# Optimization experiments

Hardware: AMD Instinct MI355X
Metric: run time of the kernel (lower is better)

## Reference

```python
import jax, jax.numpy as jnp
import numpy as np

N = 4096            # nodes
LMAX = 6
NUM_COEF = (LMAX + 1) ** 2   # 49 SH coefficients
RES = 18            # S2 grid resolution (lat = lon = 18)
C = 128             # num_channels


def setup_inputs() -> dict:
    key = jax.random.key(0)
    k1, k2, k3, k4 = jax.random.split(key, 4)
    return {
        "inputs": jax.random.normal(k1, (N, NUM_COEF, 2 * C), dtype=jnp.float32),
        "scalars": jax.random.normal(k2, (N, 3 * C), dtype=jnp.float32),
        # SO3Grid projection matrices (precomputed SH-basis grids in the real module)
        "to_grid_mat": jax.random.normal(k3, (RES, RES, NUM_COEF), dtype=jnp.float32) / np.sqrt(NUM_COEF).astype(np.float32),
        "from_grid_mat": jax.random.normal(k4, (RES, RES, NUM_COEF), dtype=jnp.float32) / np.float32(RES),
    }


def reference(inputs, scalars, to_grid_mat, from_grid_mat):
    # inputs:  [N, (lmax+1)^2, 2C]; scalars: [N, 3C]
    n, k, c2 = inputs.shape
    s = scalars[:, None, :]                       # [N, 1, 3C]
    # Type-0 path part 1: SwiGLU on first 2C scalars -> [N, 1, C]
    a, b = jnp.split(s[..., :c2], 2, axis=-1)
    output_scalars = jax.nn.silu(a) * b
    # Type-0 path part 2: sigmoid gate on last C scalars -> [N, 1, C]
    gate_scalars = jax.nn.sigmoid(s[..., c2:])
    # Type-L path: project to S2 grid -> [N, RES, RES, 2C]
    x_grid = jnp.einsum('pqi,nic->npqc', to_grid_mat, inputs)
    # chunk-multiply gating (self tensor product) -> [N, RES, RES, C]
    x1, x2 = jnp.split(x_grid, 2, axis=-1)
    x_grid = x1 * x2
    # project back to SH coefficients -> [N, (lmax+1)^2, C]
    output_vectors = jnp.einsum('pqi,npqc->nic', from_grid_mat, x_grid)
    output_vectors = output_vectors * gate_scalars
    # merge: add SwiGLU scalars onto the l=0 component
    return output_vectors.at[:, 0:1, :].add(output_scalars)
```

## Files before the change

### kernel.cpp

```cpp
#include <hip/hip_runtime.h>


#define KC    49
#define PQ    324
#define NPX   12544
#define OUTK  6272
#define NTILE 11
#define TROWS 325
#define TCOLS 68
#define FROWS 50
#define FCOLS 356
#define TTOT  (TROWS * TCOLS)
#define FTOT  (FROWS * FCOLS)
#define WTOT  (TTOT + FTOT)
#define WPAD  39904

typedef __attribute__((ext_vector_type(8)))  short bf16x8;
typedef __attribute__((ext_vector_type(4)))  short bf16x4;
typedef __attribute__((ext_vector_type(16))) float f32x16;
typedef __attribute__((ext_vector_type(4)))  unsigned int u32x4;

__device__ __forceinline__ unsigned int cvtpk_bf16(float lo, float hi) {
    unsigned int r;
    asm("v_cvt_pk_bf16_f32 %0, %1, %2" : "=v"(r) : "v"(lo), "v"(hi));
    return r;
}
__device__ __forceinline__ unsigned short f2bf(float f) {
    unsigned u = __builtin_bit_cast(unsigned, f);
    return (unsigned short)((u + 0x7FFFu + ((u >> 16) & 1u)) >> 16);
}
__device__ __forceinline__ bf16x8 ld8(const unsigned short* p) {
    const bf16x4 lo = *(const bf16x4*)p;
    const bf16x4 hi = *(const bf16x4*)(p + 4);
    bf16x8 r;
    r[0] = lo[0]; r[1] = lo[1]; r[2] = lo[2]; r[3] = lo[3];
    r[4] = hi[0]; r[5] = hi[1]; r[6] = hi[2]; r[7] = hi[3];
    return r;
}
__device__ __forceinline__ void load_ch(const float* xp, int xi, int st, int hb, float* buf) {
#pragma unroll
    for (int j = 0; j < 8; ++j) {
        const int i = 16 * st + 8 * hb + j;
        buf[j] = (i < KC) ? xp[128 * xi + (size_t)i * 256] : 0.0f;
    }
}
__device__ __forceinline__ bf16x8 cvt_ch(const float* buf) {
    u32x4 d;
#pragma unroll
    for (int p = 0; p < 4; ++p) d[p] = cvtpk_bf16(buf[2 * p], buf[2 * p + 1]);
    return __builtin_bit_cast(bf16x8, d);
}

__global__ void prep_kernel(const float* __restrict__ Tg, const float* __restrict__ Fg,
                            unsigned short* __restrict__ W)
{
    const int idx = blockIdx.x * 256 + threadIdx.x;
    if (idx < TTOT) {
        const int r = idx / TCOLS, i = idx % TCOLS;
        const float v = (r < PQ && i < KC) ? Tg[r * KC + i] : 0.0f;
        W[idx] = f2bf(v);
    } else if (idx < WPAD) {
        float v = 0.0f;
        if (idx < WTOT) {
            const int idx2 = idx - TTOT;
            const int k = idx2 / FCOLS, p = idx2 % FCOLS;
            if (k < KC && p < PQ) v = Fg[p * KC + k];
        }
        W[idx] = f2bf(v);
    }
}

__global__ __launch_bounds__(512, 4)
void s2_fused(const float* __restrict__ X,
              const float* __restrict__ S,
              const unsigned short* __restrict__ W,
              float* __restrict__ out,
              int nit)
{
    __shared__ __align__(16) unsigned short lds[WPAD];

    const int tid = threadIdx.x;
    for (int idx = tid; idx < WPAD / 8; idx += 512) {
        const u32x4 v = *(const u32x4*)(W + (size_t)idx * 8);
        *(u32x4*)(lds + (size_t)idx * 8) = v;
    }
    __syncthreads();

    const int w  = tid >> 6;
    const int l  = tid & 63;
    const int cl = l & 31;
    const int hb = l >> 5;
    const int cs = w >> 1;
    const int nw = w & 1;

    const unsigned short* tw  = lds;
    const unsigned short* fw0 = lds + TTOT + (size_t)cl * FCOLS;
    const unsigned short* fw1 = lds + TTOT + (size_t)min(cl + 32, KC) * FCOLS;

    const int nbase = blockIdx.x * (2 * nit) + nw;

    for (int it = 0; it < nit; ++it) {
        const int n = nbase + 2 * it;

        const float* xp = X + (size_t)n * NPX + 32 * cs + cl;
        const float* sp = S + (size_t)n * 384 + 32 * cs + cl;
        const float sraw0 = sp[0], sraw1 = sp[128], sraw2 = sp[256];
        const float sg  = 1.0f / (1.0f + __expf(-sraw2));
        const float osc = (sraw0 / (1.0f + __expf(-sraw0))) * sraw1;

        bf16x8 bx[2][4];
        {
            float rA[8], rB[8];
            load_ch(xp, 0, 0, hb, rA);
            load_ch(xp, 1, 0, hb, rB);
            bx[0][0] = cvt_ch(rA); load_ch(xp, 0, 1, hb, rA);
            bx[1][0] = cvt_ch(rB); load_ch(xp, 1, 1, hb, rB);
            bx[0][1] = cvt_ch(rA); load_ch(xp, 0, 2, hb, rA);
            bx[1][1] = cvt_ch(rB); load_ch(xp, 1, 2, hb, rB);
            bx[0][2] = cvt_ch(rA); load_ch(xp, 0, 3, hb, rA);
            bx[1][2] = cvt_ch(rB); load_ch(xp, 1, 3, hb, rB);
            bx[0][3] = cvt_ch(rA);
            bx[1][3] = cvt_ch(rB);
        }

        f32x16 accO0, accO1;
#pragma unroll
        for (int r = 0; r < 16; ++r) { accO0[r] = 0.0f; accO1[r] = 0.0f; }

        for (int t = 0; t < NTILE; ++t) {
            const int trow = min(32 * t + cl, 324);
            const unsigned short* twt = tw + trow * TCOLS + 8 * hb;

            f32x16 ac0, ac1;
#pragma unroll
            for (int r = 0; r < 16; ++r) { ac0[r] = 0.0f; ac1[r] = 0.0f; }

            {
                const bf16x8 ta0 = ld8(twt);
                const bf16x8 ta1 = ld8(twt + 16);
                ac0 = __builtin_amdgcn_mfma_f32_32x32x16_bf16(ta0, bx[0][0], ac0, 0, 0, 0);
                ac1 = __builtin_amdgcn_mfma_f32_32x32x16_bf16(ta0, bx[1][0], ac1, 0, 0, 0);
                ac0 = __builtin_amdgcn_mfma_f32_32x32x16_bf16(ta1, bx[0][1], ac0, 0, 0, 0);
                ac1 = __builtin_amdgcn_mfma_f32_32x32x16_bf16(ta1, bx[1][1], ac1, 0, 0, 0);
            }
            {
                const bf16x8 ta2 = ld8(twt + 32);
                const bf16x8 ta3 = ld8(twt + 48);
                ac0 = __builtin_amdgcn_mfma_f32_32x32x16_bf16(ta2, bx[0][2], ac0, 0, 0, 0);
                ac1 = __builtin_amdgcn_mfma_f32_32x32x16_bf16(ta2, bx[1][2], ac1, 0, 0, 0);
                ac0 = __builtin_amdgcn_mfma_f32_32x32x16_bf16(ta3, bx[0][3], ac0, 0, 0, 0);
                ac1 = __builtin_amdgcn_mfma_f32_32x32x16_bf16(ta3, bx[1][3], ac1, 0, 0, 0);
            }

            unsigned int q0 = cvtpk_bf16(ac0[0]  * ac1[0],  ac0[1]  * ac1[1]);
            unsigned int q1 = cvtpk_bf16(ac0[2]  * ac1[2],  ac0[3]  * ac1[3]);
            unsigned int q2 = cvtpk_bf16(ac0[4]  * ac1[4],  ac0[5]  * ac1[5]);
            unsigned int q3 = cvtpk_bf16(ac0[6]  * ac1[6],  ac0[7]  * ac1[7]);
            unsigned int q4 = cvtpk_bf16(ac0[8]  * ac1[8],  ac0[9]  * ac1[9]);
            unsigned int q5 = cvtpk_bf16(ac0[10] * ac1[10], ac0[11] * ac1[11]);
            unsigned int q6 = cvtpk_bf16(ac0[12] * ac1[12], ac0[13] * ac1[13]);
            unsigned int q7 = cvtpk_bf16(ac0[14] * ac1[14], ac0[15] * ac1[15]);

            asm("v_permlane32_swap_b32 %0, %1" : "+v"(q0), "+v"(q2));
            asm("v_permlane32_swap_b32 %0, %1" : "+v"(q1), "+v"(q3));
            asm("v_permlane32_swap_b32 %0, %1" : "+v"(q4), "+v"(q6));
            asm("v_permlane32_swap_b32 %0, %1" : "+v"(q5), "+v"(q7));
            u32x4 b0v, b1v;
            b0v[0] = q0; b0v[1] = q1; b0v[2] = q2; b0v[3] = q3;
            b1v[0] = q4; b1v[1] = q5; b1v[2] = q6; b1v[3] = q7;
            const bf16x8 bg0 = __builtin_bit_cast(bf16x8, b0v);
            const bf16x8 bg1 = __builtin_bit_cast(bf16x8, b1v);

            const int fcol = 32 * t + 8 * hb;
            {
                const bf16x8 fa00 = ld8(fw0 + fcol);
                const bf16x8 fa10 = ld8(fw1 + fcol);
                accO0 = __builtin_amdgcn_mfma_f32_32x32x16_bf16(fa00, bg0, accO0, 0, 0, 0);
                accO1 = __builtin_amdgcn_mfma_f32_32x32x16_bf16(fa10, bg0, accO1, 0, 0, 0);
            }
            {
                const bf16x8 fa01 = ld8(fw0 + fcol + 16);
                const bf16x8 fa11 = ld8(fw1 + fcol + 16);
                accO0 = __builtin_amdgcn_mfma_f32_32x32x16_bf16(fa01, bg1, accO0, 0, 0, 0);
                accO1 = __builtin_amdgcn_mfma_f32_32x32x16_bf16(fa11, bg1, accO1, 0, 0, 0);
            }
        }

        float* op = out + (size_t)n * OUTK + 32 * cs + cl;
#pragma unroll
        for (int r = 0; r < 16; ++r) {
            const int k0 = (r & 3) + 8 * (r >> 2) + 4 * hb;
            float v = sg * accO0[r];
            if (k0 == 0) v += osc;
            op[(size_t)k0 * 128] = v;
            const int k1 = 32 + k0;
            if (k1 < KC) op[(size_t)k1 * 128] = sg * accO1[r];
        }
    }
}

extern "C" void kernel_launch(void* const* d_in, const int* in_sizes, int n_in,
                              void* d_out, int out_size, void* d_ws, size_t ws_size,
                              hipStream_t stream) {
    const float* inputs  = (const float*)d_in[0];
    const float* scalars = (const float*)d_in[1];
    const float* Tg      = (const float*)d_in[2];
    const float* Fg      = (const float*)d_in[3];
    float* outp          = (float*)d_out;

    unsigned short* W = (unsigned short*)d_ws;

    const int N = in_sizes[1] / 384;
    hipLaunchKernelGGL(prep_kernel, dim3((WPAD + 255) / 256), dim3(256), 0, stream,
                       Tg, Fg, W);

    const int nit  = 4;
    const int grid = N / (2 * nit);
    hipLaunchKernelGGL(s2_fused, dim3(grid), dim3(512), 0, stream,
                       inputs, scalars, W, outp, nit);
}
```

Baseline: 98.46 us.

## Prefetch next to-grid tile, stagger tile order per wave, relax launch bounds

Software-pipelines the to-grid weight LDS loads by loading the next tile's A fragments during the current tile's MFMAs. Each wave starts at a different tile offset (rotating over 11 tiles) so LDS bank accesses are spread across waves. It also deepens the input load pipeline to four buffers and seeds the first MFMA from a zero vector passed as a runtime argument. Launch bounds drop from 4 to 2 waves-per-SIMD minimum, which frees more registers but may lower occupancy.

```diff
diff --git a/kernel.cpp b/kernel.cpp
--- a/kernel.cpp
+++ b/kernel.cpp
@@ -70,12 +70,13 @@
     }
 }
 
-__global__ __launch_bounds__(512, 4)
+__global__ __launch_bounds__(512, 2)
 void s2_fused(const float* __restrict__ X,
               const float* __restrict__ S,
               const unsigned short* __restrict__ W,
               float* __restrict__ out,
-              int nit)
+              int nit,
+              float fzero)
 {
     __shared__ __align__(16) unsigned short lds[WPAD];
 
@@ -97,6 +98,18 @@
     const unsigned short* fw0 = lds + TTOT + (size_t)cl * FCOLS;
     const unsigned short* fw1 = lds + TTOT + (size_t)min(cl + 32, KC) * FCOLS;
 
+    f32x16 Z;
+#pragma unroll
+    for (int r = 0; r < 16; ++r) Z[r] = fzero;
+
+    int ttc = (3 * w + (int)blockIdx.x) % NTILE;
+
+    const unsigned short* twt0 = tw + (size_t)min(32 * ttc + cl, 324) * TCOLS + 8 * hb;
+    bf16x8 tc0 = ld8(twt0);
+    bf16x8 tc1 = ld8(twt0 + 16);
+    bf16x8 tc2 = ld8(twt0 + 32);
+    bf16x8 tc3 = ld8(twt0 + 48);
+
     const int nbase = blockIdx.x * (2 * nit) + nw;
 
     for (int it = 0; it < nit; ++it) {
@@ -110,17 +123,19 @@
 
         bf16x8 bx[2][4];
         {
-            float rA[8], rB[8];
-            load_ch(xp, 0, 0, hb, rA);
-            load_ch(xp, 1, 0, hb, rB);
-            bx[0][0] = cvt_ch(rA); load_ch(xp, 0, 1, hb, rA);
-            bx[1][0] = cvt_ch(rB); load_ch(xp, 1, 1, hb, rB);
-            bx[0][1] = cvt_ch(rA); load_ch(xp, 0, 2, hb, rA);
-            bx[1][1] = cvt_ch(rB); load_ch(xp, 1, 2, hb, rB);
-            bx[0][2] = cvt_ch(rA); load_ch(xp, 0, 3, hb, rA);
-            bx[1][2] = cvt_ch(rB); load_ch(xp, 1, 3, hb, rB);
-            bx[0][3] = cvt_ch(rA);
-            bx[1][3] = cvt_ch(rB);
+            float r0[8], r1[8], r2[8], r3[8];
+            load_ch(xp, 0, 0, hb, r0);
+            load_ch(xp, 1, 0, hb, r1);
+            load_ch(xp, 0, 1, hb, r2);
+            load_ch(xp, 1, 1, hb, r3);
+            bx[0][0] = cvt_ch(r0); load_ch(xp, 0, 2, hb, r0);
+            bx[1][0] = cvt_ch(r1); load_ch(xp, 1, 2, hb, r1);
+            bx[0][1] = cvt_ch(r2); load_ch(xp, 0, 3, hb, r2);
+            bx[1][1] = cvt_ch(r3); load_ch(xp, 1, 3, hb, r3);
+            bx[0][2] = cvt_ch(r0);
+            bx[1][2] = cvt_ch(r1);
+            bx[0][3] = cvt_ch(r2);
+            bx[1][3] = cvt_ch(r3);
         }
 
         f32x16 accO0, accO1;
@@ -128,29 +143,28 @@
         for (int r = 0; r < 16; ++r) { accO0[r] = 0.0f; accO1[r] = 0.0f; }
 
         for (int t = 0; t < NTILE; ++t) {
-            const int trow = min(32 * t + cl, 324);
-            const unsigned short* twt = tw + trow * TCOLS + 8 * hb;
+            const int ttn = (ttc == NTILE - 1) ? 0 : ttc + 1;
+            const unsigned short* twtN = tw + (size_t)min(32 * ttn + cl, 324) * TCOLS + 8 * hb;
+            const bf16x8 nc0 = ld8(twtN);
+            const bf16x8 nc1 = ld8(twtN + 16);
+            const bf16x8 nc2 = ld8(twtN + 32);
+            const bf16x8 nc3 = ld8(twtN + 48);
 
             f32x16 ac0, ac1;
-#pragma unroll
-            for (int r = 0; r < 16; ++r) { ac0[r] = 0.0f; ac1[r] = 0.0f; }
-
-            {
-                const bf16x8 ta0 = ld8(twt);
-                const bf16x8 ta1 = ld8(twt + 16);
-                ac0 = __builtin_amdgcn_mfma_f32_32x32x16_bf16(ta0, bx[0][0], ac0, 0, 0, 0);
-                ac1 = __builtin_amdgcn_mfma_f32_32x32x16_bf16(ta0, bx[1][0], ac1, 0, 0, 0);
-                ac0 = __builtin_amdgcn_mfma_f32_32x32x16_bf16(ta1, bx[0][1], ac0, 0, 0, 0);
-                ac1 = __builtin_amdgcn_mfma_f32_32x32x16_bf16(ta1, bx[1][1], ac1, 0, 0, 0);
-            }
-            {
-                const bf16x8 ta2 = ld8(twt + 32);
-                const bf16x8 ta3 = ld8(twt + 48);
-                ac0 = __builtin_amdgcn_mfma_f32_32x32x16_bf16(ta2, bx[0][2], ac0, 0, 0, 0);
-                ac1 = __builtin_amdgcn_mfma_f32_32x32x16_bf16(ta2, bx[1][2], ac1, 0, 0, 0);
-                ac0 = __builtin_amdgcn_mfma_f32_32x32x16_bf16(ta3, bx[0][3], ac0, 0, 0, 0);
-                ac1 = __builtin_amdgcn_mfma_f32_32x32x16_bf16(ta3, bx[1][3], ac1, 0, 0, 0);
-            }
+            ac0 = __builtin_amdgcn_mfma_f32_32x32x16_bf16(tc0, bx[0][0], Z, 0, 0, 0);
+            ac1 = __builtin_amdgcn_mfma_f32_32x32x16_bf16(tc0, bx[1][0], Z, 0, 0, 0);
+            ac0 = __builtin_amdgcn_mfma_f32_32x32x16_bf16(tc1, bx[0][1], ac0, 0, 0, 0);
+            ac1 = __builtin_amdgcn_mfma_f32_32x32x16_bf16(tc1, bx[1][1], ac1, 0, 0, 0);
+            ac0 = __builtin_amdgcn_mfma_f32_32x32x16_bf16(tc2, bx[0][2], ac0, 0, 0, 0);
+            ac1 = __builtin_amdgcn_mfma_f32_32x32x16_bf16(tc2, bx[1][2], ac1, 0, 0, 0);
+            ac0 = __builtin_amdgcn_mfma_f32_32x32x16_bf16(tc3, bx[0][3], ac0, 0, 0, 0);
+            ac1 = __builtin_amdgcn_mfma_f32_32x32x16_bf16(tc3, bx[1][3], ac1, 0, 0, 0);
+
+            const int fcol = 32 * ttc + 8 * hb;
+            const bf16x8 fa00 = ld8(fw0 + fcol);
+            const bf16x8 fa01 = ld8(fw0 + fcol + 16);
+            const bf16x8 fa10 = ld8(fw1 + fcol);
+            const bf16x8 fa11 = ld8(fw1 + fcol + 16);
 
             unsigned int q0 = cvtpk_bf16(ac0[0]  * ac1[0],  ac0[1]  * ac1[1]);
             unsigned int q1 = cvtpk_bf16(ac0[2]  * ac1[2],  ac0[3]  * ac1[3]);
@@ -171,19 +185,13 @@
             const bf16x8 bg0 = __builtin_bit_cast(bf16x8, b0v);
             const bf16x8 bg1 = __builtin_bit_cast(bf16x8, b1v);
 
-            const int fcol = 32 * t + 8 * hb;
-            {
-                const bf16x8 fa00 = ld8(fw0 + fcol);
-                const bf16x8 fa10 = ld8(fw1 + fcol);
-                accO0 = __builtin_amdgcn_mfma_f32_32x32x16_bf16(fa00, bg0, accO0, 0, 0, 0);
-                accO1 = __builtin_amdgcn_mfma_f32_32x32x16_bf16(fa10, bg0, accO1, 0, 0, 0);
-            }
-            {
-                const bf16x8 fa01 = ld8(fw0 + fcol + 16);
-                const bf16x8 fa11 = ld8(fw1 + fcol + 16);
-                accO0 = __builtin_amdgcn_mfma_f32_32x32x16_bf16(fa01, bg1, accO0, 0, 0, 0);
-                accO1 = __builtin_amdgcn_mfma_f32_32x32x16_bf16(fa11, bg1, accO1, 0, 0, 0);
-            }
+            accO0 = __builtin_amdgcn_mfma_f32_32x32x16_bf16(fa00, bg0, accO0, 0, 0, 0);
+            accO1 = __builtin_amdgcn_mfma_f32_32x32x16_bf16(fa10, bg0, accO1, 0, 0, 0);
+            accO0 = __builtin_amdgcn_mfma_f32_32x32x16_bf16(fa01, bg1, accO0, 0, 0, 0);
+            accO1 = __builtin_amdgcn_mfma_f32_32x32x16_bf16(fa11, bg1, accO1, 0, 0, 0);
+
+            tc0 = nc0; tc1 = nc1; tc2 = nc2; tc3 = nc3;
+            ttc = ttn;
         }
 
         float* op = out + (size_t)n * OUTK + 32 * cs + cl;
@@ -217,5 +225,5 @@
     const int nit  = 4;
     const int grid = N / (2 * nit);
     hipLaunchKernelGGL(s2_fused, dim3(grid), dim3(512), 0, stream,
-                       inputs, scalars, W, outp, nit);
-}
+                       inputs, scalars, W, outp, nit, 0.0f);
+}
```

After: 95.21 us. -3.3%, faster.
